# Performance work log

Measured on AMD Instinct MI355X. Metric: run time of the kernel, lower is better.

The kernel has to match this reference:

```python
import jax, jax.numpy as jnp
import numpy as np

L, B, F, H, C = 1024, 8, 256, 8, 32  # seq, batch, feature_dim, heads, head_size
EPS = 1e-5


def setup_inputs() -> dict:
    key = jax.random.key(0)
    ks = jax.random.split(key, 12)
    s = 0.02
    f32 = jnp.float32
    return {
        "features": jax.random.normal(ks[0], (L, B, F), f32),
        "ln_g": jnp.ones((F,), f32),
        "ln_b": jnp.zeros((F,), f32),
        "Wq": jax.random.normal(ks[1], (F, H * C), f32) * s,
        "bq": jnp.zeros((H * C,), f32),
        "Wk": jax.random.normal(ks[2], (F, H * C), f32) * s,
        "bk": jnp.zeros((H * C,), f32),
        "Wv": jax.random.normal(ks[3], (F, H * C), f32) * s,
        "bv": jnp.zeros((H * C,), f32),
        "Wb": jax.random.normal(ks[4], (F, H), f32) * s,
        "bb": jnp.zeros((H,), f32),
        "Wg": jax.random.normal(ks[5], (F, H * C), f32) * s,
        "bg": jnp.zeros((H * C,), f32),
        "Wo": jax.random.normal(ks[6], (H * C, F), f32) * s,
        "bo": jnp.zeros((F,), f32),
    }


def _layernorm(x, g, b):
    mu = jnp.mean(x, axis=-1, keepdims=True)
    var = jnp.var(x, axis=-1, keepdims=True)
    return (x - mu) * jax.lax.rsqrt(var + EPS) * g + b


def reference(features, ln_g, ln_b, Wq, bq, Wk, bk, Wv, bv, Wb, bb, Wg, bg, Wo, bo):
    # features: (L, B, F) -- sequence-first layout (see einsum axis analysis)
    x = _layernorm(features, ln_g, ln_b)
    q = (x @ Wq + bq).reshape(L, B, H, C)  # (Lq, B, H, C)
    k = (x @ Wk + bk).reshape(L, B, H, C)  # (Lk, B, H, C)
    v = (x @ Wv + bv).reshape(L, B, H, C)
    bias = x @ Wb + bb                      # (Lk, B, H) per-key-position bias
    gate = jax.nn.sigmoid(x @ Wg + bg).reshape(L, B, H, C)

    sq_c = 1.0 / np.sqrt(C).astype(np.float32)
    # logits[q, b, k, h]
    logits = jnp.einsum('qbhc,kbhc->qbkh', q, k) * sq_c
    logits = logits + jnp.transpose(bias, (1, 0, 2))[None]  # (1, B, Lk, H)
    w = jax.nn.softmax(logits, axis=2)                      # softmax over keys
    attn = jnp.einsum('qbkh,kbhc->qbhc', w, v)              # (Lq, B, H, C)
    out = (attn * gate).reshape(L, B, H * C)
    return out @ Wo + bo                                    # (L, B, F)
```

## Files before the change

kernel.cpp:

```cpp
#include <hip/hip_runtime.h>
#include <math.h>

#define LQ 1024
#define BB 8
#define FF 256
#define HH 8
#define CC 32
#define MROWS (LQ*BB)
static constexpr float EPSV  = 1e-5f;
static constexpr float LOG2E = 1.4426950408889634f;
static constexpr float C1    = 0.17677669529663687f * 1.4426950408889634f;

typedef short  short8  __attribute__((ext_vector_type(8)));
typedef short  short4v __attribute__((ext_vector_type(4)));
typedef float  float4v __attribute__((ext_vector_type(4)));

__device__ inline unsigned short f2bf(float f) {
    unsigned int u = __builtin_bit_cast(unsigned int, f);
    u += 0x7FFFu + ((u >> 16) & 1u);
    return (unsigned short)(u >> 16);
}
__device__ inline float bf2f(unsigned short h) {
    unsigned int u = ((unsigned int)h) << 16;
    return __builtin_bit_cast(float, u);
}
__device__ inline unsigned int cvt_pk_bf16(float a, float b) {
    unsigned int r;
    asm("v_cvt_pk_bf16_f32 %0, %1, %2" : "=v"(r) : "v"(a), "v"(b));
    return r;
}

__global__ __launch_bounds__(256)
void prep_ln_kernel(const float* __restrict__ x, const float* __restrict__ g,
                    const float* __restrict__ bln,
                    const float* __restrict__ Wq, const float* __restrict__ Wk,
                    const float* __restrict__ Wv, const float* __restrict__ Wg,
                    const float* __restrict__ Wo, const float* __restrict__ Wb,
                    const float* __restrict__ bq, const float* __restrict__ bk,
                    const float* __restrict__ bv, const float* __restrict__ bg,
                    unsigned short* __restrict__ xb, unsigned short* __restrict__ wt,
                    unsigned short* __restrict__ wto,
                    float* __restrict__ bcomb, float* __restrict__ wbt) {
    int bid = blockIdx.x;
    if (bid < 2048) {
        int wid  = threadIdx.x >> 6;
        int lane = threadIdx.x & 63;
        int row  = bid * 4 + wid;
        float4 v = reinterpret_cast<const float4*>(x + (size_t)row * FF)[lane];
        float s  = v.x + v.y + v.z + v.w;
        float sq = v.x*v.x + v.y*v.y + v.z*v.z + v.w*v.w;
        #pragma unroll
        for (int m = 1; m < 64; m <<= 1) {
            s  += __shfl_xor(s,  m);
            sq += __shfl_xor(sq, m);
        }
        float mean = s * (1.0f / FF);
        float var  = sq * (1.0f / FF) - mean * mean;
        float rstd = rsqrtf(var + EPSV);
        float4 gg = reinterpret_cast<const float4*>(g)[lane];
        float4 bv4 = reinterpret_cast<const float4*>(bln)[lane];
        short4v o;
        o[0] = (short)f2bf((v.x - mean) * rstd * gg.x + bv4.x);
        o[1] = (short)f2bf((v.y - mean) * rstd * gg.y + bv4.y);
        o[2] = (short)f2bf((v.z - mean) * rstd * gg.z + bv4.z);
        o[3] = (short)f2bf((v.w - mean) * rstd * gg.w + bv4.w);
        *reinterpret_cast<short4v*>(xb + (size_t)row * FF + lane * 4) = o;
    } else if (bid < 2112) {
        int k0 = (bid - 2048) * 4;
        int nl = threadIdx.x;
        const float* Ws[5] = {Wq, Wk, Wv, Wg, Wo};
        #pragma unroll
        for (int sel = 0; sel < 5; ++sel) {
            const float* W = Ws[sel];
            short4v o;
            #pragma unroll
            for (int j = 0; j < 4; ++j)
                o[j] = (short)f2bf(W[(size_t)(k0 + j) * 256 + nl]);
            unsigned short* dst = (sel < 4)
                ? (wt + ((size_t)sel * 256 + nl) * 256 + k0)
                : (wto + (size_t)nl * 256 + k0);
            *reinterpret_cast<short4v*>(dst) = o;
        }
        if (k0 == 0) {
            bcomb[nl]       = bq[nl];
            bcomb[256 + nl] = bk[nl];
            bcomb[512 + nl] = bv[nl];
            bcomb[768 + nl] = bg[nl];
        }
    } else {
        int nl = threadIdx.x;
        #pragma unroll
        for (int hh = 0; hh < 8; ++hh)
            wbt[hh * 256 + nl] = Wb[(size_t)nl * 8 + hh];
    }
}

__global__ __launch_bounds__(256)
void qkvg_fused_kernel(const unsigned short* __restrict__ A,
                       const unsigned short* __restrict__ Bt,
                       const float* __restrict__ bcomb,
                       const float* __restrict__ wbt,
                       const float* __restrict__ bbv,
                       unsigned short* __restrict__ outq,
                       float* __restrict__ outb) {
    __shared__ unsigned short Asb[128 * 64];
    __shared__ unsigned short Bsb[128 * 64];
    int bid = blockIdx.x;
    int tid = threadIdx.x;

    if (bid >= 512) {
        int idx = (bid - 512) * 256 + tid;
        int row = idx >> 3, hh = idx & 7;
        const unsigned short* xr = A + (size_t)row * 256;
        const float* wr = wbt + hh * 256;
        float s = 0.f;
        #pragma unroll 4
        for (int i = 0; i < 32; ++i) {
            short8 x8 = *reinterpret_cast<const short8*>(xr + i * 8);
            float4 wa = *reinterpret_cast<const float4*>(wr + i * 8);
            float4 wb2 = *reinterpret_cast<const float4*>(wr + i * 8 + 4);
            s += bf2f((unsigned short)x8[0]) * wa.x + bf2f((unsigned short)x8[1]) * wa.y
               + bf2f((unsigned short)x8[2]) * wa.z + bf2f((unsigned short)x8[3]) * wa.w;
            s += bf2f((unsigned short)x8[4]) * wb2.x + bf2f((unsigned short)x8[5]) * wb2.y
               + bf2f((unsigned short)x8[6]) * wb2.z + bf2f((unsigned short)x8[7]) * wb2.w;
        }
        outb[idx] = s + bbv[hh];
        return;
    }

    int lane = tid & 63;
    int w    = tid >> 6;
    int wm   = w >> 1, wn = w & 1;
    int l15  = lane & 15, lg = lane >> 4;
    int bm   = (bid & 63) * 128;
    int bn   = (bid >> 6) * 128;

    float4v acc[4][4];
    #pragma unroll
    for (int i = 0; i < 4; ++i)
        #pragma unroll
        for (int j = 0; j < 4; ++j)
            acc[i][j] = (float4v){0.f, 0.f, 0.f, 0.f};

    for (int k0 = 0; k0 < 256; k0 += 64) {
        __syncthreads();
        #pragma unroll
        for (int p = 0; p < 4; ++p) {
            int off  = p * 256 + tid;
            int row  = off >> 3;
            int slot = off & 7;
            int ps   = (slot ^ (row & 7)) * 8;
            short8 a8 = *reinterpret_cast<const short8*>(
                A + (size_t)(bm + row) * 256 + k0 + slot * 8);
            *reinterpret_cast<short8*>(Asb + row * 64 + ps) = a8;
            short8 b8 = *reinterpret_cast<const short8*>(
                Bt + (size_t)(bn + row) * 256 + k0 + slot * 8);
            *reinterpret_cast<short8*>(Bsb + row * 64 + ps) = b8;
        }
        __syncthreads();
        #pragma unroll
        for (int kh = 0; kh < 2; ++kh) {
            int slot = kh * 4 + lg;
            short8 af[4], bf[4];
            #pragma unroll
            for (int mf = 0; mf < 4; ++mf) {
                int row = wm * 64 + mf * 16 + l15;
                af[mf] = *reinterpret_cast<const short8*>(
                    Asb + row * 64 + ((slot ^ (row & 7)) * 8));
            }
            #pragma unroll
            for (int nf = 0; nf < 4; ++nf) {
                int row = wn * 64 + nf * 16 + l15;
                bf[nf] = *reinterpret_cast<const short8*>(
                    Bsb + row * 64 + ((slot ^ (row & 7)) * 8));
            }
            #pragma unroll
            for (int mf = 0; mf < 4; ++mf)
                #pragma unroll
                for (int nf = 0; nf < 4; ++nf)
                    acc[mf][nf] = __builtin_amdgcn_mfma_f32_16x16x32_bf16(
                        bf[nf], af[mf], acc[mf][nf], 0, 0, 0);
        }
    }

    int sel = bn >> 8;
    unsigned short* outp = outq + (size_t)sel * MROWS * 256;
    #pragma unroll
    for (int mf = 0; mf < 4; ++mf) {
        int m = bm + wm * 64 + mf * 16 + l15;
        #pragma unroll
        for (int nf = 0; nf < 4; ++nf) {
            int nglob = bn + wn * 64 + nf * 16 + lg * 4;
            float4 b4 = *reinterpret_cast<const float4*>(bcomb + nglob);
            float v0 = acc[mf][nf][0] + b4.x;
            float v1 = acc[mf][nf][1] + b4.y;
            float v2 = acc[mf][nf][2] + b4.z;
            float v3 = acc[mf][nf][3] + b4.w;
            if (sel == 3) {
                v0 = 1.0f / (1.0f + __expf(-v0));
                v1 = 1.0f / (1.0f + __expf(-v1));
                v2 = 1.0f / (1.0f + __expf(-v2));
                v3 = 1.0f / (1.0f + __expf(-v3));
            }
            uint2 st;
            st.x = cvt_pk_bf16(v0, v1);
            st.y = cvt_pk_bf16(v2, v3);
            *reinterpret_cast<uint2*>(outp + (size_t)m * 256 + (nglob & 255)) = st;
        }
    }
}

__global__ __launch_bounds__(512)
void attn_mfma_kernel(const unsigned short* __restrict__ qkvg,
                      const float* __restrict__ biasp,
                      unsigned short* __restrict__ ag) {
    __shared__ unsigned short ks[64][40];
    __shared__ unsigned short vt[32 * 64];
    __shared__ unsigned short ps[8][16 * 64];
    __shared__ float bias_s[64];
    const unsigned short* qb = qkvg;
    const unsigned short* kb = qkvg + (size_t)MROWS * 256;
    const unsigned short* vb = qkvg + (size_t)MROWS * 256 * 2;
    const unsigned short* gb = qkvg + (size_t)MROWS * 256 * 3;

    int tid  = threadIdx.x;
    int lane = tid & 63;
    int w    = tid >> 6;
    int l15  = lane & 15, lg = lane >> 4;
    int bh   = blockIdx.y;
    int b    = bh >> 3, h = bh & 7;
    int qrow0 = blockIdx.x * 128 + w * 16;

    bool isK = tid < 256;
    int krow = tid >> 2, kc8 = (tid & 3) * 8;
    int tv = tid - 256, cv = (tv & 7) * 4, kp = tv >> 3;

    short8 qf = *reinterpret_cast<const short8*>(
        qb + ((size_t)(qrow0 + l15) * 8 + b) * 256 + h * 32 + lg * 8);

    float lsum = 0.f;
    float4v oacc0 = {0.f, 0.f, 0.f, 0.f}, oacc1 = {0.f, 0.f, 0.f, 0.f};

    short8 kreg; short4v v0r, v1r; float breg = 0.f;
    if (isK) {
        kreg = *reinterpret_cast<const short8*>(
            kb + ((size_t)krow * 8 + b) * 256 + h * 32 + kc8);
        if (tid < 64) breg = biasp[(size_t)tid * 64 + b * 8 + h] * LOG2E;
    } else {
        const unsigned short* vp =
            vb + ((size_t)(2 * kp) * 8 + b) * 256 + h * 32 + cv;
        v0r = *reinterpret_cast<const short4v*>(vp);
        v1r = *reinterpret_cast<const short4v*>(vp + 8 * 256);
    }

    for (int c0 = 0; c0 < LQ; c0 += 64) {
        __syncthreads();
        if (isK) {
            *reinterpret_cast<short8*>(&ks[krow][kc8]) = kreg;
            if (tid < 64) bias_s[tid] = breg;
        } else {
            #pragma unroll
            for (int j = 0; j < 4; ++j) {
                int c = cv + j;
                unsigned int pk = (unsigned int)(unsigned short)v0r[j] |
                                  ((unsigned int)(unsigned short)v1r[j] << 16);
                int slot = kp >> 2;
                int off  = c * 64 + ((slot ^ (c & 7)) * 8) + ((2 * kp) & 7);
                *reinterpret_cast<unsigned int*>(&vt[off]) = pk;
            }
        }
        __syncthreads();
        int cn = c0 + 64;
        if (cn < LQ) {
            if (isK) {
                kreg = *reinterpret_cast<const short8*>(
                    kb + ((size_t)(cn + krow) * 8 + b) * 256 + h * 32 + kc8);
                if (tid < 64) breg = biasp[(size_t)(cn + tid) * 64 + b * 8 + h] * LOG2E;
            } else {
                const unsigned short* vp =
                    vb + ((size_t)(cn + 2 * kp) * 8 + b) * 256 + h * 32 + cv;
                v0r = *reinterpret_cast<const short4v*>(vp);
                v1r = *reinterpret_cast<const short4v*>(vp + 8 * 256);
            }
        }

        __builtin_amdgcn_s_setprio(1);
        float4v sc[4];
        #pragma unroll
        for (int kt = 0; kt < 4; ++kt) {
            short8 kf = *reinterpret_cast<const short8*>(&ks[kt * 16 + l15][lg * 8]);
            sc[kt] = __builtin_amdgcn_mfma_f32_16x16x32_bf16(
                kf, qf, (float4v){0.f, 0.f, 0.f, 0.f}, 0, 0, 0);
        }
        __builtin_amdgcn_s_setprio(0);

        float psum = 0.f;
        #pragma unroll
        for (int kt = 0; kt < 4; ++kt) {
            float4v b4 = *reinterpret_cast<const float4v*>(&bias_s[kt * 16 + lg * 4]);
            float p0 = __builtin_amdgcn_exp2f(fmaf(sc[kt][0], C1, b4[0]));
            float p1 = __builtin_amdgcn_exp2f(fmaf(sc[kt][1], C1, b4[1]));
            float p2 = __builtin_amdgcn_exp2f(fmaf(sc[kt][2], C1, b4[2]));
            float p3 = __builtin_amdgcn_exp2f(fmaf(sc[kt][3], C1, b4[3]));
            psum += (p0 + p1) + (p2 + p3);
            uint2 pk;
            pk.x = cvt_pk_bf16(p0, p1);
            pk.y = cvt_pk_bf16(p2, p3);
            int slot = kt * 2 + (lg >> 1);
            int off  = l15 * 64 + ((slot ^ (l15 & 7)) * 8) + (lg & 1) * 4;
            *reinterpret_cast<uint2*>(&ps[w][off]) = pk;
        }
        psum += __shfl_xor(psum, 16);
        psum += __shfl_xor(psum, 32);
        lsum += psum;

        __builtin_amdgcn_s_setprio(1);
        #pragma unroll
        for (int kh = 0; kh < 2; ++kh) {
            int slot = kh * 4 + lg;
            short8 pf = *reinterpret_cast<const short8*>(
                &ps[w][l15 * 64 + ((slot ^ (l15 & 7)) * 8)]);
            int c0r = l15, c1r = 16 + l15;
            short8 vf0 = *reinterpret_cast<const short8*>(
                &vt[c0r * 64 + ((slot ^ (c0r & 7)) * 8)]);
            short8 vf1 = *reinterpret_cast<const short8*>(
                &vt[c1r * 64 + ((slot ^ (c1r & 7)) * 8)]);
            oacc0 = __builtin_amdgcn_mfma_f32_16x16x32_bf16(vf0, pf, oacc0, 0, 0, 0);
            oacc1 = __builtin_amdgcn_mfma_f32_16x16x32_bf16(vf1, pf, oacc1, 0, 0, 0);
        }
        __builtin_amdgcn_s_setprio(0);
    }

    float linv = 1.0f / lsum;
    size_t base = ((size_t)(qrow0 + l15) * 8 + b) * 256 + h * 32;
    #pragma unroll
    for (int ct = 0; ct < 2; ++ct) {
        int c0 = ct * 16 + lg * 4;
        float4v oa = ct ? oacc1 : oacc0;
        short4v g4 = *reinterpret_cast<const short4v*>(gb + base + c0);
        float v0 = oa[0] * linv * bf2f((unsigned short)g4[0]);
        float v1 = oa[1] * linv * bf2f((unsigned short)g4[1]);
        float v2 = oa[2] * linv * bf2f((unsigned short)g4[2]);
        float v3 = oa[3] * linv * bf2f((unsigned short)g4[3]);
        uint2 st;
        st.x = cvt_pk_bf16(v0, v1);
        st.y = cvt_pk_bf16(v2, v3);
        *reinterpret_cast<uint2*>(ag + base + c0) = st;
    }
}

__global__ __launch_bounds__(256)
void gemm_out_kernel(const unsigned short* __restrict__ A,
                     const unsigned short* __restrict__ Bt,
                     const float* __restrict__ bias,
                     float* __restrict__ Cout) {
    __shared__ unsigned short Asb[64 * 64];
    __shared__ unsigned short Bsb[128 * 64];
    int tid  = threadIdx.x;
    int lane = tid & 63;
    int w    = tid >> 6;
    int l15  = lane & 15, lg = lane >> 4;
    int bm   = blockIdx.x * 64;
    int bn   = blockIdx.y * 128;

    float4v acc[4][2];
    #pragma unroll
    for (int i = 0; i < 4; ++i)
        #pragma unroll
        for (int j = 0; j < 2; ++j)
            acc[i][j] = (float4v){0.f, 0.f, 0.f, 0.f};

    for (int k0 = 0; k0 < 256; k0 += 64) {
        __syncthreads();
        #pragma unroll
        for (int p = 0; p < 2; ++p) {
            int off = p * 256 + tid;
            int row = off >> 3, slot = off & 7;
            short8 a8 = *reinterpret_cast<const short8*>(
                A + (size_t)(bm + row) * 256 + k0 + slot * 8);
            *reinterpret_cast<short8*>(Asb + row * 64 + ((slot ^ (row & 7)) * 8)) = a8;
        }
        #pragma unroll
        for (int p = 0; p < 4; ++p) {
            int off = p * 256 + tid;
            int row = off >> 3, slot = off & 7;
            short8 b8 = *reinterpret_cast<const short8*>(
                Bt + (size_t)(bn + row) * 256 + k0 + slot * 8);
            *reinterpret_cast<short8*>(Bsb + row * 64 + ((slot ^ (row & 7)) * 8)) = b8;
        }
        __syncthreads();
        #pragma unroll
        for (int kh = 0; kh < 2; ++kh) {
            int slot = kh * 4 + lg;
            short8 af[4], bf[2];
            #pragma unroll
            for (int mf = 0; mf < 4; ++mf) {
                int row = mf * 16 + l15;
                af[mf] = *reinterpret_cast<const short8*>(
                    Asb + row * 64 + ((slot ^ (row & 7)) * 8));
            }
            #pragma unroll
            for (int nf = 0; nf < 2; ++nf) {
                int row = w * 32 + nf * 16 + l15;
                bf[nf] = *reinterpret_cast<const short8*>(
                    Bsb + row * 64 + ((slot ^ (row & 7)) * 8));
            }
            #pragma unroll
            for (int mf = 0; mf < 4; ++mf)
                #pragma unroll
                for (int nf = 0; nf < 2; ++nf)
                    acc[mf][nf] = __builtin_amdgcn_mfma_f32_16x16x32_bf16(
                        bf[nf], af[mf], acc[mf][nf], 0, 0, 0);
        }
    }
    #pragma unroll
    for (int mf = 0; mf < 4; ++mf) {
        int m = bm + mf * 16 + l15;
        #pragma unroll
        for (int nf = 0; nf < 2; ++nf) {
            int c0 = bn + w * 32 + nf * 16 + lg * 4;
            float4 b4 = *reinterpret_cast<const float4*>(bias + c0);
            float4 o;
            o.x = acc[mf][nf][0] + b4.x;
            o.y = acc[mf][nf][1] + b4.y;
            o.z = acc[mf][nf][2] + b4.z;
            o.w = acc[mf][nf][3] + b4.w;
            *reinterpret_cast<float4*>(Cout + (size_t)m * 256 + c0) = o;
        }
    }
}

extern "C" void kernel_launch(void* const* d_in, const int* in_sizes, int n_in,
                              void* d_out, int out_size, void* d_ws, size_t ws_size,
                              hipStream_t stream) {
    (void)in_sizes; (void)n_in; (void)out_size; (void)ws_size;
    const float* features = (const float*)d_in[0];
    const float* ln_g = (const float*)d_in[1];
    const float* ln_b = (const float*)d_in[2];
    const float* Wq = (const float*)d_in[3];
    const float* bq = (const float*)d_in[4];
    const float* Wk = (const float*)d_in[5];
    const float* bk = (const float*)d_in[6];
    const float* Wv = (const float*)d_in[7];
    const float* bv = (const float*)d_in[8];
    const float* Wb = (const float*)d_in[9];
    const float* bbv = (const float*)d_in[10];
    const float* Wg = (const float*)d_in[11];
    const float* bg = (const float*)d_in[12];
    const float* Wo = (const float*)d_in[13];
    const float* bo = (const float*)d_in[14];
    float* out = (float*)d_out;

    char* wsb = (char*)d_ws;
    unsigned short* xb    = (unsigned short*)(wsb);
    unsigned short* wt    = (unsigned short*)(wsb + 4194304);
    unsigned short* wto   = (unsigned short*)(wsb + 4718592);
    float*          bcomb = (float*)(wsb + 4849664);
    float*          wbt   = (float*)(wsb + 4853760);
    unsigned short* qkvg  = (unsigned short*)(wsb + 4861952);
    float*          biasb = (float*)(wsb + 21639168);
    unsigned short* agb   = (unsigned short*)(wsb + 21901312);

    prep_ln_kernel<<<dim3(2113), dim3(256), 0, stream>>>(
        features, ln_g, ln_b, Wq, Wk, Wv, Wg, Wo, Wb,
        bq, bk, bv, bg, xb, wt, wto, bcomb, wbt);
    qkvg_fused_kernel<<<dim3(768), dim3(256), 0, stream>>>(
        xb, wt, bcomb, wbt, bbv, qkvg, biasb);
    attn_mfma_kernel<<<dim3(8, 64), dim3(512), 0, stream>>>(
        qkvg, biasb, agb);
    gemm_out_kernel<<<dim3(128, 2), dim3(256), 0, stream>>>(
        agb, wto, bo, out);
}
```

Before: 62.24 us.

## Use direct global-to-LDS loads in GEMMs and widen attention key tile to 128

Both projection GEMMs now stage A and B tiles with global_load_lds (16-byte direct-to-LDS loads). The XOR swizzle moves to the global source address so that the LDS writes stay contiguous per wave. This avoids the round trip through VGPRs. The attention kernel processes 128 keys per iteration instead of 64, with every thread loading both K and V rather than splitting the block into K and V halves. That halves the number of loop iterations and barriers, at the cost of more LDS and more score registers per wave.

```diff
diff --git a/kernel.cpp b/kernel.cpp
--- a/kernel.cpp
+++ b/kernel.cpp
@@ -28,6 +28,11 @@
     unsigned int r;
     asm("v_cvt_pk_bf16_f32 %0, %1, %2" : "=v"(r) : "v"(a), "v"(b));
     return r;
+}
+__device__ __forceinline__ void gl_lds16(const unsigned short* g, unsigned short* l) {
+    __builtin_amdgcn_global_load_lds(
+        (const __attribute__((address_space(1))) void*)g,
+        (__attribute__((address_space(3))) void*)l, 16, 0, 0);
 }
 
 __global__ __launch_bounds__(256)
@@ -145,17 +150,13 @@
     for (int k0 = 0; k0 < 256; k0 += 64) {
         __syncthreads();
         #pragma unroll
-        for (int p = 0; p < 4; ++p) {
-            int off  = p * 256 + tid;
-            int row  = off >> 3;
-            int slot = off & 7;
-            int ps   = (slot ^ (row & 7)) * 8;
-            short8 a8 = *reinterpret_cast<const short8*>(
-                A + (size_t)(bm + row) * 256 + k0 + slot * 8);
-            *reinterpret_cast<short8*>(Asb + row * 64 + ps) = a8;
-            short8 b8 = *reinterpret_cast<const short8*>(
-                Bt + (size_t)(bn + row) * 256 + k0 + slot * 8);
-            *reinterpret_cast<short8*>(Bsb + row * 64 + ps) = b8;
+        for (int j = 0; j < 4; ++j) {
+            int c = w * 4 + j;
+            int u = c * 64 + lane;
+            int row = u >> 3, slot = u & 7;
+            size_t gsw = (size_t)row * 256 + k0 + ((slot ^ (row & 7)) * 8);
+            gl_lds16(A + (size_t)bm * 256 + gsw, Asb + c * 512);
+            gl_lds16(Bt + (size_t)bn * 256 + gsw, Bsb + c * 512);
         }
         __syncthreads();
         #pragma unroll
@@ -214,10 +215,10 @@
 void attn_mfma_kernel(const unsigned short* __restrict__ qkvg,
                       const float* __restrict__ biasp,
                       unsigned short* __restrict__ ag) {
-    __shared__ unsigned short ks[64][40];
-    __shared__ unsigned short vt[32 * 64];
-    __shared__ unsigned short ps[8][16 * 64];
-    __shared__ float bias_s[64];
+    __shared__ unsigned short ksl[128][40];
+    __shared__ unsigned short vt[32 * 128];
+    __shared__ unsigned short ps[8][16 * 128];
+    __shared__ float bias_s[128];
     const unsigned short* qb = qkvg;
     const unsigned short* kb = qkvg + (size_t)MROWS * 256;
     const unsigned short* vb = qkvg + (size_t)MROWS * 256 * 2;
@@ -231,9 +232,8 @@
     int b    = bh >> 3, h = bh & 7;
     int qrow0 = blockIdx.x * 128 + w * 16;
 
-    bool isK = tid < 256;
     int krow = tid >> 2, kc8 = (tid & 3) * 8;
-    int tv = tid - 256, cv = (tv & 7) * 4, kp = tv >> 3;
+    int cv = (tid & 7) * 4, kp = tid >> 3;
 
     short8 qf = *reinterpret_cast<const short8*>(
         qb + ((size_t)(qrow0 + l15) * 8 + b) * 256 + h * 32 + lg * 8);
@@ -242,53 +242,46 @@
     float4v oacc0 = {0.f, 0.f, 0.f, 0.f}, oacc1 = {0.f, 0.f, 0.f, 0.f};
 
     short8 kreg; short4v v0r, v1r; float breg = 0.f;
-    if (isK) {
+    {
         kreg = *reinterpret_cast<const short8*>(
             kb + ((size_t)krow * 8 + b) * 256 + h * 32 + kc8);
-        if (tid < 64) breg = biasp[(size_t)tid * 64 + b * 8 + h] * LOG2E;
-    } else {
         const unsigned short* vp =
             vb + ((size_t)(2 * kp) * 8 + b) * 256 + h * 32 + cv;
         v0r = *reinterpret_cast<const short4v*>(vp);
         v1r = *reinterpret_cast<const short4v*>(vp + 8 * 256);
-    }
-
-    for (int c0 = 0; c0 < LQ; c0 += 64) {
-        __syncthreads();
-        if (isK) {
-            *reinterpret_cast<short8*>(&ks[krow][kc8]) = kreg;
-            if (tid < 64) bias_s[tid] = breg;
-        } else {
-            #pragma unroll
-            for (int j = 0; j < 4; ++j) {
-                int c = cv + j;
-                unsigned int pk = (unsigned int)(unsigned short)v0r[j] |
-                                  ((unsigned int)(unsigned short)v1r[j] << 16);
-                int slot = kp >> 2;
-                int off  = c * 64 + ((slot ^ (c & 7)) * 8) + ((2 * kp) & 7);
-                *reinterpret_cast<unsigned int*>(&vt[off]) = pk;
-            }
-        }
-        __syncthreads();
-        int cn = c0 + 64;
+        if (tid < 128) breg = biasp[(size_t)tid * 64 + b * 8 + h] * LOG2E;
+    }
+
+    for (int c0 = 0; c0 < LQ; c0 += 128) {
+        __syncthreads();
+        *reinterpret_cast<short8*>(&ksl[krow][kc8]) = kreg;
+        #pragma unroll
+        for (int j = 0; j < 4; ++j) {
+            int c = cv + j;
+            unsigned int pk = (unsigned int)(unsigned short)v0r[j] |
+                              ((unsigned int)(unsigned short)v1r[j] << 16);
+            int slot = kp >> 2;
+            int off  = c * 128 + ((slot ^ (c & 7)) * 8) + ((2 * kp) & 7);
+            *reinterpret_cast<unsigned int*>(&vt[off]) = pk;
+        }
+        if (tid < 128) bias_s[tid] = breg;
+        __syncthreads();
+        int cn = c0 + 128;
         if (cn < LQ) {
-            if (isK) {
-                kreg = *reinterpret_cast<const short8*>(
-                    kb + ((size_t)(cn + krow) * 8 + b) * 256 + h * 32 + kc8);
-                if (tid < 64) breg = biasp[(size_t)(cn + tid) * 64 + b * 8 + h] * LOG2E;
-            } else {
-                const unsigned short* vp =
-                    vb + ((size_t)(cn + 2 * kp) * 8 + b) * 256 + h * 32 + cv;
-                v0r = *reinterpret_cast<const short4v*>(vp);
-                v1r = *reinterpret_cast<const short4v*>(vp + 8 * 256);
-            }
+            kreg = *reinterpret_cast<const short8*>(
+                kb + ((size_t)(cn + krow) * 8 + b) * 256 + h * 32 + kc8);
+            const unsigned short* vp =
+                vb + ((size_t)(cn + 2 * kp) * 8 + b) * 256 + h * 32 + cv;
+            v0r = *reinterpret_cast<const short4v*>(vp);
+            v1r = *reinterpret_cast<const short4v*>(vp + 8 * 256);
+            if (tid < 128) breg = biasp[(size_t)(cn + tid) * 64 + b * 8 + h] * LOG2E;
         }
 
         __builtin_amdgcn_s_setprio(1);
-        float4v sc[4];
-        #pragma unroll
-        for (int kt = 0; kt < 4; ++kt) {
-            short8 kf = *reinterpret_cast<const short8*>(&ks[kt * 16 + l15][lg * 8]);
+        float4v sc[8];
+        #pragma unroll
+        for (int kt = 0; kt < 8; ++kt) {
+            short8 kf = *reinterpret_cast<const short8*>(&ksl[kt * 16 + l15][lg * 8]);
             sc[kt] = __builtin_amdgcn_mfma_f32_16x16x32_bf16(
                 kf, qf, (float4v){0.f, 0.f, 0.f, 0.f}, 0, 0, 0);
         }
@@ -296,7 +289,7 @@
 
         float psum = 0.f;
         #pragma unroll
-        for (int kt = 0; kt < 4; ++kt) {
+        for (int kt = 0; kt < 8; ++kt) {
             float4v b4 = *reinterpret_cast<const float4v*>(&bias_s[kt * 16 + lg * 4]);
             float p0 = __builtin_amdgcn_exp2f(fmaf(sc[kt][0], C1, b4[0]));
             float p1 = __builtin_amdgcn_exp2f(fmaf(sc[kt][1], C1, b4[1]));
@@ -307,7 +300,7 @@
             pk.x = cvt_pk_bf16(p0, p1);
             pk.y = cvt_pk_bf16(p2, p3);
             int slot = kt * 2 + (lg >> 1);
-            int off  = l15 * 64 + ((slot ^ (l15 & 7)) * 8) + (lg & 1) * 4;
+            int off  = l15 * 128 + ((slot ^ (l15 & 7)) * 8) + (lg & 1) * 4;
             *reinterpret_cast<uint2*>(&ps[w][off]) = pk;
         }
         psum += __shfl_xor(psum, 16);
@@ -316,15 +309,15 @@
 
         __builtin_amdgcn_s_setprio(1);
         #pragma unroll
-        for (int kh = 0; kh < 2; ++kh) {
+        for (int kh = 0; kh < 4; ++kh) {
             int slot = kh * 4 + lg;
             short8 pf = *reinterpret_cast<const short8*>(
-                &ps[w][l15 * 64 + ((slot ^ (l15 & 7)) * 8)]);
+                &ps[w][l15 * 128 + ((slot ^ (l15 & 7)) * 8)]);
             int c0r = l15, c1r = 16 + l15;
             short8 vf0 = *reinterpret_cast<const short8*>(
-                &vt[c0r * 64 + ((slot ^ (c0r & 7)) * 8)]);
+                &vt[c0r * 128 + ((slot ^ (c0r & 7)) * 8)]);
             short8 vf1 = *reinterpret_cast<const short8*>(
-                &vt[c1r * 64 + ((slot ^ (c1r & 7)) * 8)]);
+                &vt[c1r * 128 + ((slot ^ (c1r & 7)) * 8)]);
             oacc0 = __builtin_amdgcn_mfma_f32_16x16x32_bf16(vf0, pf, oacc0, 0, 0, 0);
             oacc1 = __builtin_amdgcn_mfma_f32_16x16x32_bf16(vf1, pf, oacc1, 0, 0, 0);
         }
@@ -373,20 +366,20 @@
     for (int k0 = 0; k0 < 256; k0 += 64) {
         __syncthreads();
         #pragma unroll
-        for (int p = 0; p < 2; ++p) {
-            int off = p * 256 + tid;
-            int row = off >> 3, slot = off & 7;
-            short8 a8 = *reinterpret_cast<const short8*>(
-                A + (size_t)(bm + row) * 256 + k0 + slot * 8);
-            *reinterpret_cast<short8*>(Asb + row * 64 + ((slot ^ (row & 7)) * 8)) = a8;
-        }
-        #pragma unroll
-        for (int p = 0; p < 4; ++p) {
-            int off = p * 256 + tid;
-            int row = off >> 3, slot = off & 7;
-            short8 b8 = *reinterpret_cast<const short8*>(
-                Bt + (size_t)(bn + row) * 256 + k0 + slot * 8);
-            *reinterpret_cast<short8*>(Bsb + row * 64 + ((slot ^ (row & 7)) * 8)) = b8;
+        for (int j = 0; j < 2; ++j) {
+            int c = w * 2 + j;
+            int u = c * 64 + lane;
+            int row = u >> 3, slot = u & 7;
+            gl_lds16(A + (size_t)(bm + row) * 256 + k0 + ((slot ^ (row & 7)) * 8),
+                     Asb + c * 512);
+        }
+        #pragma unroll
+        for (int j = 0; j < 4; ++j) {
+            int c = w * 4 + j;
+            int u = c * 64 + lane;
+            int row = u >> 3, slot = u & 7;
+            gl_lds16(Bt + (size_t)(bn + row) * 256 + k0 + ((slot ^ (row & 7)) * 8),
+                     Bsb + c * 512);
         }
         __syncthreads();
         #pragma unroll
```

Result: faster. 59.38 us (median of 2 runs) (-4.6%).
